# Kernel optimization log

Measured on AMD Instinct MI355X. Metric: run time of the kernel, lower is better.

Reference implementation:

```python
import jax, jax.numpy as jnp
import numpy as np

N_EMBD = 1024
N_HEAD = 16
HEAD_SIZE = N_EMBD // N_HEAD  # 64

def setup_inputs() -> dict:
    key = jax.random.key(0)
    ks = jax.random.split(key, 6)
    B, T, C, H, S = 2, 2048, N_EMBD, N_HEAD, HEAD_SIZE
    sc = 1.0 / np.sqrt(C)
    x = jax.random.normal(ks[0], (B, T, C), dtype=jnp.float32)
    # stacked per-head projection weights (no bias), [H, C, S]
    Wq = jax.random.normal(ks[1], (H, C, S), dtype=jnp.float32) * sc
    Wk = jax.random.normal(ks[2], (H, C, S), dtype=jnp.float32) * sc
    Wv = jax.random.normal(ks[3], (H, C, S), dtype=jnp.float32) * sc
    Wp = jax.random.normal(ks[4], (C, C), dtype=jnp.float32) * sc
    bp = jax.random.normal(ks[5], (C,), dtype=jnp.float32) * 0.01
    return {"x": x, "Wq": Wq, "Wk": Wk, "Wv": Wv, "Wp": Wp, "bp": bp}

def reference(x, Wq, Wk, Wv, Wp, bp):
    # Eval-mode forward (dropout = identity), default non-flash path.
    B, T, C = x.shape
    H, _, S = Wq.shape
    q = jnp.einsum('btc,hcs->bhts', x, Wq)
    k = jnp.einsum('btc,hcs->bhts', x, Wk)
    v = jnp.einsum('btc,hcs->bhts', x, Wv)
    att = jnp.einsum('bhts,bhus->bhtu', q, k) * (1.0 / np.sqrt(S))
    causal = jnp.tril(jnp.ones((T, T), dtype=bool))
    att = jnp.where(causal[None, None], att, -jnp.inf)
    att = jax.nn.softmax(att, axis=-1)
    y = jnp.einsum('bhtu,bhus->bhts', att, v)
    # concat heads along feature dim (head-major), then output projection
    y = y.transpose(0, 2, 1, 3).reshape(B, T, H * S)
    return y @ Wp.T + bp
```

## Files before the change

### kernel.cpp

```cpp
#include <hip/hip_runtime.h>
#include <hip/hip_bf16.h>
#include <cmath>

typedef __attribute__((ext_vector_type(8))) short bf16x8;
typedef __attribute__((ext_vector_type(4))) float f32x4;
typedef __attribute__((ext_vector_type(16))) float f32x16;

__device__ __forceinline__ unsigned short f2bf(float f) {
    union { float f; unsigned int i; } c; c.f = f;
    unsigned int i = c.i;
    unsigned int r = i + 0x7FFF + ((i >> 16) & 1);
    return (unsigned short)(r >> 16);
}

__device__ __forceinline__ float fast_exp2(float x) {
    float r;
    asm("v_exp_f32 %0, %1" : "=v"(r) : "v"(x));
    return r;
}

__device__ __forceinline__ void gload_lds16(const unsigned short* g, unsigned short* l) {
    __builtin_amdgcn_global_load_lds((const __attribute__((address_space(1))) unsigned int*)g,
                                     (__attribute__((address_space(3))) unsigned int*)l, 16, 0, 0);
}

__device__ __forceinline__ float bperm_f(int srclane, float v) {
    return __int_as_float(__builtin_amdgcn_ds_bpermute(srclane << 2, __float_as_int(v)));
}

__global__ void k_cvt(const float* __restrict__ src, unsigned short* __restrict__ dst, int n4) {
    int i = blockIdx.x * blockDim.x + threadIdx.x;
    if (i < n4) {
        float4 v = reinterpret_cast<const float4*>(src)[i];
        ushort4 o;
        o.x = f2bf(v.x); o.y = f2bf(v.y); o.z = f2bf(v.z); o.w = f2bf(v.w);
        reinterpret_cast<ushort4*>(dst)[i] = o;
    }
}

__global__ void k_cvt_wt(const float* __restrict__ Wq, const float* __restrict__ Wk,
                         const float* __restrict__ Wv, unsigned short* __restrict__ Wt) {
    __shared__ unsigned short lt[64][72];
    int bid = blockIdx.x;
    int ct  = bid & 15;
    int h   = (bid >> 4) & 15;
    int sec = bid >> 8;
    const float* W = (sec == 0) ? Wq : ((sec == 1) ? Wk : Wv);
    int t = threadIdx.x;
    #pragma unroll
    for (int q = 0; q < 4; q++) {
        int id = t + q * 256;
        int c  = id >> 4;
        int s4 = (id & 15) * 4;
        float4 v = *reinterpret_cast<const float4*>(&W[((size_t)(h * 1024) + (ct * 64 + c)) * 64 + s4]);
        lt[s4 + 0][c] = f2bf(v.x);
        lt[s4 + 1][c] = f2bf(v.y);
        lt[s4 + 2][c] = f2bf(v.z);
        lt[s4 + 3][c] = f2bf(v.w);
    }
    __syncthreads();
    #pragma unroll
    for (int q = 0; q < 2; q++) {
        int id = t + q * 256;
        int s  = id >> 3;
        int c8 = (id & 7) * 8;
        bf16x8 val = *reinterpret_cast<const bf16x8*>(&lt[s][c8]);
        int n = sec * 1024 + h * 64 + s;
        *reinterpret_cast<bf16x8*>(&Wt[(size_t)n * 1024 + ct * 64 + c8]) = val;
    }
}

template <int MODE>
__launch_bounds__(256)
__global__ void k_gemm(const unsigned short* __restrict__ A,
                       const unsigned short* __restrict__ Bt,
                       int M, int N, int K,
                       unsigned short* __restrict__ q_nat,
                       unsigned short* __restrict__ k_nat,
                       unsigned short* __restrict__ vT,
                       float* __restrict__ out, const float* __restrict__ bp) {
    __shared__ unsigned short Asm[128][64];
    __shared__ unsigned short Bsm[128][64];
    const int nb = N >> 7;
    int cpx = gridDim.x >> 3;
    int bid = (blockIdx.x & 7) * cpx + (blockIdx.x >> 3);
    int n0 = (bid % nb) << 7;
    int m0 = (bid / nb) << 7;
    int t = threadIdx.x;
    int lane = t & 63, w = t >> 6;
    int wr = w >> 1, wc = w & 1;
    int l15 = lane & 15, lg = lane >> 4;
    int sr = lane >> 3;
    int scol = ((lane & 7) ^ sr) << 3;

    f32x4 acc[4][4];
    #pragma unroll
    for (int i = 0; i < 4; i++)
        #pragma unroll
        for (int j = 0; j < 4; j++) acc[i][j] = (f32x4){0.f, 0.f, 0.f, 0.f};

    for (int kt = 0; kt < K; kt += 64) {
        #pragma unroll
        for (int q = 0; q < 4; q++) {
            int rb = q * 32 + w * 8;
            int row = rb + sr;
            gload_lds16(&A[(size_t)(m0 + row) * K + kt + scol], &Asm[rb][0]);
            gload_lds16(&Bt[(size_t)(n0 + row) * K + kt + scol], &Bsm[rb][0]);
        }
        __syncthreads();
        bf16x8 af[4][2], bfr[4][2];
        int x15 = (l15 & 7) << 3;
        #pragma unroll
        for (int mi = 0; mi < 4; mi++) {
            int row = wr * 64 + mi * 16 + l15;
            af[mi][0] = *reinterpret_cast<const bf16x8*>(&Asm[row][(lg * 8) ^ x15]);
            af[mi][1] = *reinterpret_cast<const bf16x8*>(&Asm[row][(32 + lg * 8) ^ x15]);
        }
        #pragma unroll
        for (int nj = 0; nj < 4; nj++) {
            int row = wc * 64 + nj * 16 + l15;
            bfr[nj][0] = *reinterpret_cast<const bf16x8*>(&Bsm[row][(lg * 8) ^ x15]);
            bfr[nj][1] = *reinterpret_cast<const bf16x8*>(&Bsm[row][(32 + lg * 8) ^ x15]);
        }
        #pragma unroll
        for (int mi = 0; mi < 4; mi++)
            #pragma unroll
            for (int nj = 0; nj < 4; nj++) {
                acc[mi][nj] = __builtin_amdgcn_mfma_f32_16x16x32_bf16(af[mi][0], bfr[nj][0], acc[mi][nj], 0, 0, 0);
                acc[mi][nj] = __builtin_amdgcn_mfma_f32_16x16x32_bf16(af[mi][1], bfr[nj][1], acc[mi][nj], 0, 0, 0);
            }
        __syncthreads();
    }

    #pragma unroll
    for (int mi = 0; mi < 4; mi++) {
        #pragma unroll
        for (int nj = 0; nj < 4; nj++) {
            #pragma unroll
            for (int r = 0; r < 4; r++) {
                int m = m0 + wr * 64 + mi * 16 + lg * 4 + r;
                int n = n0 + wc * 64 + nj * 16 + l15;
                float v = acc[mi][nj][r];
                if (MODE == 0) {
                    int sec = n >> 10;
                    int win = n & 1023;
                    if (sec == 0) {
                        q_nat[(size_t)m * 1024 + win] = f2bf(v * 0.1803368801f);
                    } else if (sec == 1) {
                        k_nat[(size_t)m * 1024 + win] = f2bf(v);
                    } else {
                        int b = m >> 11, tt = m & 2047;
                        int h = win >> 6, s = win & 63;
                        vT[(((size_t)(b * 16 + h)) * 64 + s) * 2048 + tt] = f2bf(v);
                    }
                } else {
                    out[(size_t)m * 1024 + n] = v + bp[n];
                }
            }
        }
    }
}

__launch_bounds__(256, 4)
__global__ void k_attn(const unsigned short* __restrict__ q_nat,
                       const unsigned short* __restrict__ k_nat,
                       const unsigned short* __restrict__ vT,
                       unsigned short* __restrict__ y_bf) {
    __shared__ __align__(16) unsigned short Ks[2][2][64][64];
    __shared__ __align__(16) unsigned short Vs[2][2][64][64];
    __shared__ float cm[2][64], cl[2][64];
    const int T = 2048, H = 16;
    int bid = blockIdx.x;
    int bh = bid & 31;
    int qi = 31 - (bid >> 5);
    int h = bh & 15, b = bh >> 4;
    int t = threadIdx.x;
    int lane = t & 63, w = t >> 6;
    int pr = w >> 1, rg = w & 1;
    int l31 = lane & 31, hi = lane >> 5;
    int warp_q0 = qi * 64 + rg * 32;
    int qg = warp_q0 + l31;

    int n0 = (qi >> 1) + 1;
    int nS = pr ? ((qi + 1) >> 1) : n0;

    const unsigned short* kbase = k_nat + (size_t)(b * T) * 1024 + h * 64;
    const unsigned short* vbase = vT + ((size_t)(b * H + h) * 64) * 2048;

    int sxor = ((lane & 7) ^ (lane >> 3)) << 3;

    auto STAGE = [&](int j, int buf) {
        #pragma unroll
        for (int r = 0; r < 4; r++) {
            int rb = r * 16 + rg * 8;
            int grow = rb + (lane >> 3);
            gload_lds16(kbase + (size_t)(j * 64 + grow) * 1024 + sxor, &Ks[pr][buf][rb][0]);
            gload_lds16(vbase + (size_t)grow * 2048 + j * 64 + sxor, &Vs[pr][buf][rb][0]);
        }
    };

    bf16x8 qf[4];
    #pragma unroll
    for (int tt = 0; tt < 4; tt++)
        qf[tt] = *reinterpret_cast<const bf16x8*>(
            q_nat + (size_t)(b * T + qg) * 1024 + h * 64 + tt * 16 + hi * 8);

    f32x16 acc0, acc1;
    #pragma unroll
    for (int r = 0; r < 16; r++) { acc0[r] = 0.f; acc1[r] = 0.f; }
    float m = -INFINITY, ell = 0.f;

    if (nS > 0) STAGE(pr, 0);
    __syncthreads();
    int cur = 0;

    for (int i = 0; i < n0; i++) {
        bool act = (i < nS);
        int j = pr + 2 * i;
        if (act && (i + 1 < nS)) STAGE(j + 2, cur ^ 1);

        if (act) {
            const char* kb = (const char*)&Ks[pr][cur][0][0];
            const char* vb = (const char*)&Vs[pr][cur][0][0];
            int rsw = (l31 & 7) << 4;

            f32x16 s0, s1;
            #pragma unroll
            for (int r = 0; r < 16; r++) { s0[r] = 0.f; s1[r] = 0.f; }
            __builtin_amdgcn_s_setprio(1);
            #pragma unroll
            for (int tt = 0; tt < 4; tt++) {
                int cb = (tt * 32 + hi * 16) ^ rsw;
                bf16x8 kf0 = *reinterpret_cast<const bf16x8*>(kb + l31 * 128 + cb);
                bf16x8 kf1 = *reinterpret_cast<const bf16x8*>(kb + (32 + l31) * 128 + cb);
                s0 = __builtin_amdgcn_mfma_f32_32x32x16_bf16(kf0, qf[tt], s0, 0, 0, 0);
                s1 = __builtin_amdgcn_mfma_f32_32x32x16_bf16(kf1, qf[tt], s1, 0, 0, 0);
            }
            __builtin_amdgcn_s_setprio(0);

            if (j == qi) {
                #pragma unroll
                for (int r = 0; r < 16; r++) {
                    int kvr = (r & 3) + 8 * (r >> 2) + 4 * hi + j * 64;
                    if (kvr > qg) s0[r] = -INFINITY;
                    if (kvr + 32 > qg) s1[r] = -INFINITY;
                }
            }

            float tmax = -INFINITY;
            #pragma unroll
            for (int r = 0; r < 16; r++) tmax = fmaxf(tmax, fmaxf(s0[r], s1[r]));
            tmax = fmaxf(tmax, __shfl_xor(tmax, 32, 64));

            if (!__all(tmax <= m + 11.5f)) {
                float mn = fmaxf(m, tmax);
                float scl = fast_exp2(m - mn);
                m = mn; ell *= scl;
                #pragma unroll
                for (int r = 0; r < 16; r++) {
                    float sv = bperm_f((r & 3) + 8 * (r >> 2) + 4 * hi, scl);
                    acc0[r] *= sv; acc1[r] *= sv;
                }
            }

            float rs = 0.f;
            #pragma unroll
            for (int r = 0; r < 16; r++) {
                s0[r] = fast_exp2(s0[r] - m); rs += s0[r];
                s1[r] = fast_exp2(s1[r] - m); rs += s1[r];
            }
            rs += __shfl_xor(rs, 32, 64);
            ell += rs;

            unsigned int c[16];
            #pragma unroll
            for (int i2 = 0; i2 < 8; i2++) {
                asm("v_cvt_pk_bf16_f32 %0, %1, %2" : "=v"(c[i2]) : "v"(s0[2 * i2]), "v"(s0[2 * i2 + 1]));
                asm("v_cvt_pk_bf16_f32 %0, %1, %2" : "=v"(c[8 + i2]) : "v"(s1[2 * i2]), "v"(s1[2 * i2 + 1]));
            }
            bf16x8 pa[4];
            #pragma unroll
            for (int ks = 0; ks < 4; ks++) {
                unsigned int clo0 = c[ks * 4 + 0], clo1 = c[ks * 4 + 1];
                unsigned int chi0 = c[ks * 4 + 2], chi1 = c[ks * 4 + 3];
                unsigned int pl0 = (unsigned int)__shfl_xor((int)clo0, 32, 64);
                unsigned int pl1 = (unsigned int)__shfl_xor((int)clo1, 32, 64);
                unsigned int ph0 = (unsigned int)__shfl_xor((int)chi0, 32, 64);
                unsigned int ph1 = (unsigned int)__shfl_xor((int)chi1, 32, 64);
                union { unsigned int u[4]; bf16x8 v; } fr;
                fr.u[0] = hi ? ph0 : clo0;
                fr.u[1] = hi ? ph1 : clo1;
                fr.u[2] = hi ? chi0 : pl0;
                fr.u[3] = hi ? chi1 : pl1;
                pa[ks] = fr.v;
            }

            __builtin_amdgcn_s_setprio(1);
            #pragma unroll
            for (int ks = 0; ks < 4; ks++) {
                int cb = (ks * 32 + hi * 16) ^ rsw;
                bf16x8 v0 = *reinterpret_cast<const bf16x8*>(vb + l31 * 128 + cb);
                bf16x8 v1 = *reinterpret_cast<const bf16x8*>(vb + (32 + l31) * 128 + cb);
                acc0 = __builtin_amdgcn_mfma_f32_32x32x16_bf16(pa[ks], v0, acc0, 0, 0, 0);
                acc1 = __builtin_amdgcn_mfma_f32_32x32x16_bf16(pa[ks], v1, acc1, 0, 0, 0);
            }
            __builtin_amdgcn_s_setprio(0);
        }

        __syncthreads();
        cur ^= 1;
    }

    if (hi == 0) { cm[pr][rg * 32 + l31] = m; cl[pr][rg * 32 + l31] = ell; }
    __syncthreads();

    int rowi = rg * 32 + l31;
    float m0v = cm[0][rowi], l0v = cl[0][rowi];
    float m1v = cm[1][rowi], l1v = cl[1][rowi];
    float mSt = fmaxf(m0v, m1v);
    float w0 = (m0v > -1e30f) ? fast_exp2(m0v - mSt) : 0.f;
    float w1 = (m1v > -1e30f) ? fast_exp2(m1v - mSt) : 0.f;
    float denom = 1.f / (l0v * w0 + l1v * w1);
    float myw = pr ? w1 : w0;

    float* Ocomb = (float*)&Ks[0][0][0][0];
    if (pr == 1) {
        #pragma unroll
        for (int r = 0; r < 16; r++) {
            int qr = (r & 3) + 8 * (r >> 2) + 4 * hi;
            float sB = bperm_f(qr, myw);
            Ocomb[(rg * 32 + qr) * 64 + l31] = acc0[r] * sB;
            Ocomb[(rg * 32 + qr) * 64 + 32 + l31] = acc1[r] * sB;
        }
    }
    __syncthreads();
    if (pr == 0) {
        #pragma unroll
        for (int r = 0; r < 16; r++) {
            int qr = (r & 3) + 8 * (r >> 2) + 4 * hi;
            float sA = bperm_f(qr, myw);
            float dv = bperm_f(qr, denom);
            float o0 = acc0[r] * sA + Ocomb[(rg * 32 + qr) * 64 + l31];
            float o1 = acc1[r] * sA + Ocomb[(rg * 32 + qr) * 64 + 32 + l31];
            size_t row = (size_t)(b * T + warp_q0 + qr) * 1024 + h * 64;
            y_bf[row + l31] = f2bf(o0 * dv);
            y_bf[row + 32 + l31] = f2bf(o1 * dv);
        }
    }
}

extern "C" void kernel_launch(void* const* d_in, const int* in_sizes, int n_in,
                              void* d_out, int out_size, void* d_ws, size_t ws_size,
                              hipStream_t stream) {
    const float* x  = (const float*)d_in[0];
    const float* Wq = (const float*)d_in[1];
    const float* Wk = (const float*)d_in[2];
    const float* Wv = (const float*)d_in[3];
    const float* Wp = (const float*)d_in[4];
    const float* bp = (const float*)d_in[5];
    float* out = (float*)d_out;

    char* ws = (char*)d_ws;
    unsigned short* x_bf  = (unsigned short*)(ws);
    unsigned short* Wt    = (unsigned short*)(ws + ((size_t)8  << 20));
    unsigned short* Wp_bf = (unsigned short*)(ws + ((size_t)14 << 20));
    unsigned short* q_nat = (unsigned short*)(ws + ((size_t)16 << 20));
    unsigned short* k_nat = (unsigned short*)(ws + ((size_t)24 << 20));
    unsigned short* vT    = (unsigned short*)(ws + ((size_t)32 << 20));
    unsigned short* y_bf  = (unsigned short*)(ws + ((size_t)40 << 20));

    k_cvt<<<4096, 256, 0, stream>>>(x, x_bf, 4194304 / 4);
    k_cvt<<<1024, 256, 0, stream>>>(Wp, Wp_bf, 1048576 / 4);
    k_cvt_wt<<<768, 256, 0, stream>>>(Wq, Wk, Wv, Wt);
    k_gemm<0><<<24 * 32, 256, 0, stream>>>(x_bf, Wt, 4096, 3072, 1024,
                                           q_nat, k_nat, vT, nullptr, nullptr);
    k_attn<<<1024, 256, 0, stream>>>(q_nat, k_nat, vT, y_bf);
    k_gemm<1><<<8 * 32, 256, 0, stream>>>(y_bf, Wp_bf, 4096, 1024, 1024,
                                          nullptr, nullptr, nullptr, out, bp);
}
```

Measured before the change: 124.2 us.

## Restructure attention into single-wave blocks loading K/V directly from global

Each attention block is now a single 64-lane wave handling 32 query rows, launched as 2048 blocks with an interleaved head mapping. The LDS double-buffered staging, the split of KV tiles across two wave pairs, and the cross-wave softmax merge are all removed. K and V fragments are read straight from global memory into registers. This removes barriers and LDS traffic, but each wave now reloads K/V from global or cache without pipelining and walks the full causal range serially, which lengthens the critical path for late query blocks.

New measurement: 149.1 us. 20.0% more time.

```diff
diff --git a/kernel.cpp b/kernel.cpp
--- a/kernel.cpp
+++ b/kernel.cpp
@@ -161,43 +161,24 @@
     }
 }
 
-__launch_bounds__(256, 4)
+__launch_bounds__(64, 2)
 __global__ void k_attn(const unsigned short* __restrict__ q_nat,
                        const unsigned short* __restrict__ k_nat,
                        const unsigned short* __restrict__ vT,
                        unsigned short* __restrict__ y_bf) {
-    __shared__ __align__(16) unsigned short Ks[2][2][64][64];
-    __shared__ __align__(16) unsigned short Vs[2][2][64][64];
-    __shared__ float cm[2][64], cl[2][64];
     const int T = 2048, H = 16;
-    int bid = blockIdx.x;
-    int bh = bid & 31;
-    int qi = 31 - (bid >> 5);
+    int d = blockIdx.x;
+    int bh = (d & 7) | (((d >> 3) & 3) << 3);
+    int g  = 63 - (d >> 5);
     int h = bh & 15, b = bh >> 4;
-    int t = threadIdx.x;
-    int lane = t & 63, w = t >> 6;
-    int pr = w >> 1, rg = w & 1;
+    int lane = threadIdx.x;
     int l31 = lane & 31, hi = lane >> 5;
-    int warp_q0 = qi * 64 + rg * 32;
+    int warp_q0 = g * 32;
     int qg = warp_q0 + l31;
-
-    int n0 = (qi >> 1) + 1;
-    int nS = pr ? ((qi + 1) >> 1) : n0;
+    int ntile = (warp_q0 >> 6) + 1;
 
     const unsigned short* kbase = k_nat + (size_t)(b * T) * 1024 + h * 64;
     const unsigned short* vbase = vT + ((size_t)(b * H + h) * 64) * 2048;
-
-    int sxor = ((lane & 7) ^ (lane >> 3)) << 3;
-
-    auto STAGE = [&](int j, int buf) {
-        #pragma unroll
-        for (int r = 0; r < 4; r++) {
-            int rb = r * 16 + rg * 8;
-            int grow = rb + (lane >> 3);
-            gload_lds16(kbase + (size_t)(j * 64 + grow) * 1024 + sxor, &Ks[pr][buf][rb][0]);
-            gload_lds16(vbase + (size_t)grow * 2048 + j * 64 + sxor, &Vs[pr][buf][rb][0]);
-        }
-    };
 
     bf16x8 qf[4];
     #pragma unroll
@@ -210,142 +191,106 @@
     for (int r = 0; r < 16; r++) { acc0[r] = 0.f; acc1[r] = 0.f; }
     float m = -INFINITY, ell = 0.f;
 
-    if (nS > 0) STAGE(pr, 0);
-    __syncthreads();
-    int cur = 0;
-
-    for (int i = 0; i < n0; i++) {
-        bool act = (i < nS);
-        int j = pr + 2 * i;
-        if (act && (i + 1 < nS)) STAGE(j + 2, cur ^ 1);
-
-        if (act) {
-            const char* kb = (const char*)&Ks[pr][cur][0][0];
-            const char* vb = (const char*)&Vs[pr][cur][0][0];
-            int rsw = (l31 & 7) << 4;
-
-            f32x16 s0, s1;
-            #pragma unroll
-            for (int r = 0; r < 16; r++) { s0[r] = 0.f; s1[r] = 0.f; }
-            __builtin_amdgcn_s_setprio(1);
-            #pragma unroll
-            for (int tt = 0; tt < 4; tt++) {
-                int cb = (tt * 32 + hi * 16) ^ rsw;
-                bf16x8 kf0 = *reinterpret_cast<const bf16x8*>(kb + l31 * 128 + cb);
-                bf16x8 kf1 = *reinterpret_cast<const bf16x8*>(kb + (32 + l31) * 128 + cb);
-                s0 = __builtin_amdgcn_mfma_f32_32x32x16_bf16(kf0, qf[tt], s0, 0, 0, 0);
-                s1 = __builtin_amdgcn_mfma_f32_32x32x16_bf16(kf1, qf[tt], s1, 0, 0, 0);
-            }
-            __builtin_amdgcn_s_setprio(0);
-
-            if (j == qi) {
-                #pragma unroll
-                for (int r = 0; r < 16; r++) {
-                    int kvr = (r & 3) + 8 * (r >> 2) + 4 * hi + j * 64;
-                    if (kvr > qg) s0[r] = -INFINITY;
-                    if (kvr + 32 > qg) s1[r] = -INFINITY;
-                }
-            }
-
-            float tmax = -INFINITY;
-            #pragma unroll
-            for (int r = 0; r < 16; r++) tmax = fmaxf(tmax, fmaxf(s0[r], s1[r]));
-            tmax = fmaxf(tmax, __shfl_xor(tmax, 32, 64));
-
-            if (!__all(tmax <= m + 11.5f)) {
-                float mn = fmaxf(m, tmax);
-                float scl = fast_exp2(m - mn);
-                m = mn; ell *= scl;
-                #pragma unroll
-                for (int r = 0; r < 16; r++) {
-                    float sv = bperm_f((r & 3) + 8 * (r >> 2) + 4 * hi, scl);
-                    acc0[r] *= sv; acc1[r] *= sv;
-                }
-            }
-
-            float rs = 0.f;
+    for (int j = 0; j < ntile; j++) {
+        const unsigned short* krow = kbase + (size_t)(j * 64) * 1024;
+        bf16x8 kf0[4], kf1[4];
+        #pragma unroll
+        for (int tt = 0; tt < 4; tt++) {
+            kf0[tt] = *reinterpret_cast<const bf16x8*>(krow + (size_t)l31 * 1024 + tt * 16 + hi * 8);
+            kf1[tt] = *reinterpret_cast<const bf16x8*>(krow + (size_t)(32 + l31) * 1024 + tt * 16 + hi * 8);
+        }
+        bf16x8 vf0[4], vf1[4];
+        #pragma unroll
+        for (int ks = 0; ks < 4; ks++) {
+            vf0[ks] = *reinterpret_cast<const bf16x8*>(vbase + (size_t)l31 * 2048 + j * 64 + ks * 16 + hi * 8);
+            vf1[ks] = *reinterpret_cast<const bf16x8*>(vbase + (size_t)(32 + l31) * 2048 + j * 64 + ks * 16 + hi * 8);
+        }
+
+        f32x16 s0, s1;
+        #pragma unroll
+        for (int r = 0; r < 16; r++) { s0[r] = 0.f; s1[r] = 0.f; }
+        __builtin_amdgcn_s_setprio(1);
+        #pragma unroll
+        for (int tt = 0; tt < 4; tt++) {
+            s0 = __builtin_amdgcn_mfma_f32_32x32x16_bf16(kf0[tt], qf[tt], s0, 0, 0, 0);
+            s1 = __builtin_amdgcn_mfma_f32_32x32x16_bf16(kf1[tt], qf[tt], s1, 0, 0, 0);
+        }
+        __builtin_amdgcn_s_setprio(0);
+
+        if (j == ntile - 1) {
             #pragma unroll
             for (int r = 0; r < 16; r++) {
-                s0[r] = fast_exp2(s0[r] - m); rs += s0[r];
-                s1[r] = fast_exp2(s1[r] - m); rs += s1[r];
+                int kvr = (r & 3) + 8 * (r >> 2) + 4 * hi + j * 64;
+                if (kvr > qg) s0[r] = -INFINITY;
+                if (kvr + 32 > qg) s1[r] = -INFINITY;
             }
-            rs += __shfl_xor(rs, 32, 64);
-            ell += rs;
-
-            unsigned int c[16];
+        }
+
+        float tmax = -INFINITY;
+        #pragma unroll
+        for (int r = 0; r < 16; r++) tmax = fmaxf(tmax, fmaxf(s0[r], s1[r]));
+        tmax = fmaxf(tmax, __shfl_xor(tmax, 32, 64));
+
+        if (!__all(tmax <= m + 11.5f)) {
+            float mn = fmaxf(m, tmax);
+            float scl = fast_exp2(m - mn);
+            m = mn; ell *= scl;
             #pragma unroll
-            for (int i2 = 0; i2 < 8; i2++) {
-                asm("v_cvt_pk_bf16_f32 %0, %1, %2" : "=v"(c[i2]) : "v"(s0[2 * i2]), "v"(s0[2 * i2 + 1]));
-                asm("v_cvt_pk_bf16_f32 %0, %1, %2" : "=v"(c[8 + i2]) : "v"(s1[2 * i2]), "v"(s1[2 * i2 + 1]));
+            for (int r = 0; r < 16; r++) {
+                float sv = bperm_f((r & 3) + 8 * (r >> 2) + 4 * hi, scl);
+                acc0[r] *= sv; acc1[r] *= sv;
             }
-            bf16x8 pa[4];
-            #pragma unroll
-            for (int ks = 0; ks < 4; ks++) {
-                unsigned int clo0 = c[ks * 4 + 0], clo1 = c[ks * 4 + 1];
-                unsigned int chi0 = c[ks * 4 + 2], chi1 = c[ks * 4 + 3];
-                unsigned int pl0 = (unsigned int)__shfl_xor((int)clo0, 32, 64);
-                unsigned int pl1 = (unsigned int)__shfl_xor((int)clo1, 32, 64);
-                unsigned int ph0 = (unsigned int)__shfl_xor((int)chi0, 32, 64);
-                unsigned int ph1 = (unsigned int)__shfl_xor((int)chi1, 32, 64);
-                union { unsigned int u[4]; bf16x8 v; } fr;
-                fr.u[0] = hi ? ph0 : clo0;
-                fr.u[1] = hi ? ph1 : clo1;
-                fr.u[2] = hi ? chi0 : pl0;
-                fr.u[3] = hi ? chi1 : pl1;
-                pa[ks] = fr.v;
-            }
-
-            __builtin_amdgcn_s_setprio(1);
-            #pragma unroll
-            for (int ks = 0; ks < 4; ks++) {
-                int cb = (ks * 32 + hi * 16) ^ rsw;
-                bf16x8 v0 = *reinterpret_cast<const bf16x8*>(vb + l31 * 128 + cb);
-                bf16x8 v1 = *reinterpret_cast<const bf16x8*>(vb + (32 + l31) * 128 + cb);
-                acc0 = __builtin_amdgcn_mfma_f32_32x32x16_bf16(pa[ks], v0, acc0, 0, 0, 0);
-                acc1 = __builtin_amdgcn_mfma_f32_32x32x16_bf16(pa[ks], v1, acc1, 0, 0, 0);
-            }
-            __builtin_amdgcn_s_setprio(0);
-        }
-
-        __syncthreads();
-        cur ^= 1;
-    }
-
-    if (hi == 0) { cm[pr][rg * 32 + l31] = m; cl[pr][rg * 32 + l31] = ell; }
-    __syncthreads();
-
-    int rowi = rg * 32 + l31;
-    float m0v = cm[0][rowi], l0v = cl[0][rowi];
-    float m1v = cm[1][rowi], l1v = cl[1][rowi];
-    float mSt = fmaxf(m0v, m1v);
-    float w0 = (m0v > -1e30f) ? fast_exp2(m0v - mSt) : 0.f;
-    float w1 = (m1v > -1e30f) ? fast_exp2(m1v - mSt) : 0.f;
-    float denom = 1.f / (l0v * w0 + l1v * w1);
-    float myw = pr ? w1 : w0;
-
-    float* Ocomb = (float*)&Ks[0][0][0][0];
-    if (pr == 1) {
+        }
+
+        float rs = 0.f;
         #pragma unroll
         for (int r = 0; r < 16; r++) {
-            int qr = (r & 3) + 8 * (r >> 2) + 4 * hi;
-            float sB = bperm_f(qr, myw);
-            Ocomb[(rg * 32 + qr) * 64 + l31] = acc0[r] * sB;
-            Ocomb[(rg * 32 + qr) * 64 + 32 + l31] = acc1[r] * sB;
-        }
-    }
-    __syncthreads();
-    if (pr == 0) {
-        #pragma unroll
-        for (int r = 0; r < 16; r++) {
-            int qr = (r & 3) + 8 * (r >> 2) + 4 * hi;
-            float sA = bperm_f(qr, myw);
-            float dv = bperm_f(qr, denom);
-            float o0 = acc0[r] * sA + Ocomb[(rg * 32 + qr) * 64 + l31];
-            float o1 = acc1[r] * sA + Ocomb[(rg * 32 + qr) * 64 + 32 + l31];
-            size_t row = (size_t)(b * T + warp_q0 + qr) * 1024 + h * 64;
-            y_bf[row + l31] = f2bf(o0 * dv);
-            y_bf[row + 32 + l31] = f2bf(o1 * dv);
-        }
+            s0[r] = fast_exp2(s0[r] - m); rs += s0[r];
+            s1[r] = fast_exp2(s1[r] - m); rs += s1[r];
+        }
+        rs += __shfl_xor(rs, 32, 64);
+        ell += rs;
+
+        unsigned int c[16];
+        #pragma unroll
+        for (int i2 = 0; i2 < 8; i2++) {
+            asm("v_cvt_pk_bf16_f32 %0, %1, %2" : "=v"(c[i2]) : "v"(s0[2 * i2]), "v"(s0[2 * i2 + 1]));
+            asm("v_cvt_pk_bf16_f32 %0, %1, %2" : "=v"(c[8 + i2]) : "v"(s1[2 * i2]), "v"(s1[2 * i2 + 1]));
+        }
+        bf16x8 pa[4];
+        #pragma unroll
+        for (int ks = 0; ks < 4; ks++) {
+            unsigned int clo0 = c[ks * 4 + 0], clo1 = c[ks * 4 + 1];
+            unsigned int chi0 = c[ks * 4 + 2], chi1 = c[ks * 4 + 3];
+            unsigned int pl0 = (unsigned int)__shfl_xor((int)clo0, 32, 64);
+            unsigned int pl1 = (unsigned int)__shfl_xor((int)clo1, 32, 64);
+            unsigned int ph0 = (unsigned int)__shfl_xor((int)chi0, 32, 64);
+            unsigned int ph1 = (unsigned int)__shfl_xor((int)chi1, 32, 64);
+            union { unsigned int u[4]; bf16x8 v; } fr;
+            fr.u[0] = hi ? ph0 : clo0;
+            fr.u[1] = hi ? ph1 : clo1;
+            fr.u[2] = hi ? chi0 : pl0;
+            fr.u[3] = hi ? chi1 : pl1;
+            pa[ks] = fr.v;
+        }
+
+        __builtin_amdgcn_s_setprio(1);
+        #pragma unroll
+        for (int ks = 0; ks < 4; ks++) {
+            acc0 = __builtin_amdgcn_mfma_f32_32x32x16_bf16(pa[ks], vf0[ks], acc0, 0, 0, 0);
+            acc1 = __builtin_amdgcn_mfma_f32_32x32x16_bf16(pa[ks], vf1[ks], acc1, 0, 0, 0);
+        }
+        __builtin_amdgcn_s_setprio(0);
+    }
+
+    float rinv = 1.0f / ell;
+    #pragma unroll
+    for (int r = 0; r < 16; r++) {
+        int qr = (r & 3) + 8 * (r >> 2) + 4 * hi;
+        float rv = bperm_f(qr, rinv);
+        size_t row = (size_t)(b * T + warp_q0 + qr) * 1024 + h * 64;
+        y_bf[row + l31] = f2bf(acc0[r] * rv);
+        y_bf[row + 32 + l31] = f2bf(acc1[r] * rv);
     }
 }
 
@@ -374,7 +319,7 @@
     k_cvt_wt<<<768, 256, 0, stream>>>(Wq, Wk, Wv, Wt);
     k_gemm<0><<<24 * 32, 256, 0, stream>>>(x_bf, Wt, 4096, 3072, 1024,
                                            q_nat, k_nat, vT, nullptr, nullptr);
-    k_attn<<<1024, 256, 0, stream>>>(q_nat, k_nat, vT, y_bf);
+    k_attn<<<2048, 64, 0, stream>>>(q_nat, k_nat, vT, y_bf);
     k_gemm<1><<<8 * 32, 256, 0, stream>>>(y_bf, Wp_bf, 4096, 1024, 1024,
                                           nullptr, nullptr, nullptr, out, bp);
 }
```
